# Kernel tuning notes

Hardware: AMD Instinct MI355X
Metric: run time of the kernel (lower is better)

The kernel has to match this reference:

```python
import jax, jax.numpy as jnp
import numpy as np

B, D, S, SE, H, DFF = 4, 1024, 1024, 1024, 16, 4096
DH = D // H
NUDGE = 1e-7


def norm(x):
    # x: [B, D, S]; custom layer norm: mean over (1,2), then divide by full L2 norm
    size = x.shape[1] * x.shape[2]
    mean = jnp.sum(x, axis=(1, 2)) / size
    x = x - mean[:, None, None]
    std = jnp.sqrt(jnp.sum(x * x, axis=(1, 2)))
    return x / (std[:, None, None] + NUDGE)


def mha(q_in, kv_in, Wq, Wk, Wv, Wo, causal):
    # q_in: [B, Sq, D], kv_in: [B, Sk, D]
    Bq, Sq, _ = q_in.shape
    Sk = kv_in.shape[1]
    q = (q_in @ Wq).reshape(Bq, Sq, H, DH)
    k = (kv_in @ Wk).reshape(Bq, Sk, H, DH)
    v = (kv_in @ Wv).reshape(Bq, Sk, H, DH)
    scores = jnp.einsum('bqhd,bkhd->bhqk', q, k) / jnp.sqrt(jnp.asarray(DH, q.dtype))
    if causal:
        mask = jnp.tril(jnp.ones((Sq, Sk), dtype=bool))
        scores = jnp.where(mask, scores, jnp.finfo(scores.dtype).min)
    attn = jax.nn.softmax(scores, axis=-1)
    out = jnp.einsum('bhqk,bkhd->bqhd', attn, v).reshape(Bq, Sq, D)
    return out @ Wo


def setup_inputs() -> dict:
    key = jax.random.key(0)
    ks = jax.random.split(key, 13)
    w = lambda k, sh: jax.random.normal(k, sh, dtype=jnp.float32) * 0.02
    return {
        'embedding': jax.random.normal(ks[0], (B, D, SE), dtype=jnp.float32),
        'other_inputs': jax.random.normal(ks[1], (B, D, S), dtype=jnp.float32),
        'Wq_s': w(ks[2], (D, D)), 'Wk_s': w(ks[3], (D, D)),
        'Wv_s': w(ks[4], (D, D)), 'Wo_s': w(ks[5], (D, D)),
        'Wq_c': w(ks[6], (D, D)), 'Wk_c': w(ks[7], (D, D)),
        'Wv_c': w(ks[8], (D, D)), 'Wo_c': w(ks[9], (D, D)),
        'W1': w(ks[10], (D, DFF)), 'b1': jnp.zeros((DFF,), jnp.float32),
        'W2': w(ks[11], (DFF, D)), 'b2': jnp.zeros((D,), jnp.float32),
    }


def reference(embedding, other_inputs, Wq_s, Wk_s, Wv_s, Wo_s,
              Wq_c, Wk_c, Wv_c, Wo_c, W1, b1, W2, b2):
    # tensors are [B, D, S]; attention operates on [B, S, D]
    x = other_inputs.transpose(0, 2, 1)
    sa = mha(x, x, Wq_s, Wk_s, Wv_s, Wo_s, causal=True)
    post_attention = norm(other_inputs + sa.transpose(0, 2, 1))

    pa = post_attention.transpose(0, 2, 1)
    emb = embedding.transpose(0, 2, 1)
    ca = mha(pa, emb, Wq_c, Wk_c, Wv_c, Wo_c, causal=False)
    post_embedding = norm(post_attention + ca.transpose(0, 2, 1))

    # per-token MLP (original loops over axis 2 and restacks; here fully batched)
    pe = post_embedding.transpose(0, 2, 1)  # [B, S, D]
    ff = jax.nn.relu(pe @ W1 + b1) @ W2 + b2
    return norm(post_embedding + ff.transpose(0, 2, 1))
```

## Files before the change

### kernel.cpp

```cpp
#include <hip/hip_runtime.h>
#include <cmath>

#define B_   4
#define D_   1024
#define S_   1024
#define H_   16
#define DH_  64
#define DFF_ 4096

typedef __attribute__((ext_vector_type(8))) short bf16x8;
typedef __attribute__((ext_vector_type(4))) float f32x4;

__device__ __forceinline__ unsigned short f2b(float f) {
    unsigned int u = __float_as_uint(f);
    u += 0x7fffu + ((u >> 16) & 1u);
    return (unsigned short)(u >> 16);
}

__device__ __forceinline__ void gload_lds16(const unsigned short* g, unsigned short* l) {
    __builtin_amdgcn_global_load_lds(
        (const __attribute__((address_space(1))) void*)g,
        (__attribute__((address_space(3))) void*)l, 16, 0, 0);
}

template <int BM, int BN, bool RES>
__global__ __launch_bounds__(256, 2)
void gemm_t(const unsigned short* __restrict__ A,
            const unsigned short* __restrict__ Wt,
            const float* __restrict__ bias,
            const float* __restrict__ residual,
            float* __restrict__ Cf, unsigned short* __restrict__ Cb,
            float* __restrict__ partial,
            int N, int K, int lda, int ldb, long csplit, int relu)
{
    constexpr int FM = BM / 32, FN = BN / 32;
    __shared__ unsigned short As[BM * 64];
    __shared__ unsigned short Bs[BN * 64];
    const int tid = threadIdx.x;
    const int w = tid >> 6, lane = tid & 63;
    const int quad = lane >> 4, l16 = lane & 15;
    const int m0 = blockIdx.x * BM, n0 = blockIdx.y * BN;
    const int wm = (w >> 1) * (BM / 2), wn = (w & 1) * (BN / 2);
    const int srow = lane >> 3;
    const int scol = ((lane & 7) ^ srow) * 8;

    A  += (size_t)blockIdx.z * K;
    Wt += (size_t)blockIdx.z * K;
    if (Cf) Cf += (size_t)blockIdx.z * csplit;

    f32x4 acc[FM][FN] = {};

    for (int k0 = 0; k0 < K; k0 += 64) {
#pragma unroll
        for (int i = 0; i < BM / 32; ++i) {
            const int inst = w + 4 * i;
            gload_lds16(A + (size_t)(m0 + inst * 8 + srow) * lda + k0 + scol,
                        As + inst * 512);
        }
#pragma unroll
        for (int i = 0; i < BN / 32; ++i) {
            const int inst = w + 4 * i;
            gload_lds16(Wt + (size_t)(n0 + inst * 8 + srow) * ldb + k0 + scol,
                        Bs + inst * 512);
        }
        __syncthreads();

#pragma unroll
        for (int kk = 0; kk < 2; ++kk) {
            bf16x8 af[FM], bfr[FN];
#pragma unroll
            for (int i = 0; i < FM; ++i) {
                const int r = wm + i * 16 + l16;
                af[i] = *(const bf16x8*)&As[r * 64 + (((kk * 4 + quad) ^ (r & 7)) * 8)];
            }
#pragma unroll
            for (int j = 0; j < FN; ++j) {
                const int r = wn + j * 16 + l16;
                bfr[j] = *(const bf16x8*)&Bs[r * 64 + (((kk * 4 + quad) ^ (r & 7)) * 8)];
            }
#pragma unroll
            for (int i = 0; i < FM; ++i)
#pragma unroll
                for (int j = 0; j < FN; ++j)
                    acc[i][j] = __builtin_amdgcn_mfma_f32_16x16x32_bf16(af[i], bfr[j], acc[i][j], 0, 0, 0);
        }
        __syncthreads();
    }

    float s = 0.f, ss = 0.f;
#pragma unroll
    for (int i = 0; i < FM; ++i) {
        const int grow = m0 + wm + i * 16 + quad * 4;
#pragma unroll
        for (int j = 0; j < FN; ++j) {
            const int gcol = n0 + wn + j * 16 + l16;
            const float bv = bias ? bias[gcol] : 0.f;
#pragma unroll
            for (int r = 0; r < 4; ++r) {
                float vv = acc[i][j][r] + bv;
                if (relu) vv = fmaxf(vv, 0.f);
                if constexpr (RES) {
                    vv += residual[(size_t)(grow + r) * N + gcol];
                    s += vv; ss += vv * vv;
                    Cf[(size_t)(grow + r) * N + gcol] = vv;
                } else {
                    if (Cf) Cf[(size_t)(grow + r) * N + gcol] = vv;
                    if (Cb) Cb[(size_t)(grow + r) * N + gcol] = f2b(vv);
                }
            }
        }
    }

    if constexpr (RES) {
        float* rs = (float*)As;
        float* rss = rs + 256;
        rs[tid] = s; rss[tid] = ss;
        __syncthreads();
        for (int off = 128; off > 0; off >>= 1) {
            if (tid < off) { rs[tid] += rs[tid + off]; rss[tid] += rss[tid + off]; }
            __syncthreads();
        }
        if (tid == 0) {
            constexpr int YPB = S_ / BM;
            const int b = blockIdx.x / YPB;
            const int chunk = (blockIdx.x % YPB) * gridDim.y + blockIdx.y;
            const int chunks = YPB * gridDim.y;
            partial[((size_t)b * chunks + chunk) * 2 + 0] = rs[0];
            partial[((size_t)b * chunks + chunk) * 2 + 1] = rss[0];
        }
    }
}

__global__ void reduce2_res(const float* __restrict__ pc, const float* __restrict__ res,
                            const float* __restrict__ bias, float* __restrict__ y,
                            float* __restrict__ partial)
{
    const size_t pcs = (size_t)4096 * 1024;
    const int b = blockIdx.y;
    const size_t base = (size_t)b * 1048576 + (size_t)blockIdx.x * 16384;
    float s = 0.f, ss = 0.f;
    for (int i = threadIdx.x; i < 4096; i += 256) {
        const size_t e = base + (size_t)i * 4;
        float4 v0 = *(const float4*)&pc[e];
        float4 v1 = *(const float4*)&pc[e + pcs];
        float4 rv = *(const float4*)&res[e];
        float4 bv = *(const float4*)&bias[e & 1023];
        float4 o;
        o.x = v0.x + v1.x + rv.x + bv.x;
        o.y = v0.y + v1.y + rv.y + bv.y;
        o.z = v0.z + v1.z + rv.z + bv.z;
        o.w = v0.w + v1.w + rv.w + bv.w;
        *(float4*)&y[e] = o;
        s += o.x + o.y + o.z + o.w;
        ss += o.x * o.x + o.y * o.y + o.z * o.z + o.w * o.w;
    }
    __shared__ float rs[256], rss[256];
    rs[threadIdx.x] = s; rss[threadIdx.x] = ss;
    __syncthreads();
    for (int off = 128; off > 0; off >>= 1) {
        if (threadIdx.x < off) {
            rs[threadIdx.x] += rs[threadIdx.x + off];
            rss[threadIdx.x] += rss[threadIdx.x + off];
        }
        __syncthreads();
    }
    if (threadIdx.x == 0) {
        partial[((size_t)b * 64 + blockIdx.x) * 2 + 0] = rs[0];
        partial[((size_t)b * 64 + blockIdx.x) * 2 + 1] = rss[0];
    }
}

__device__ __forceinline__ void stats_reduce(const float* __restrict__ partial,
                                             int b, int chunks, int tid,
                                             float* rs, float* rss,
                                             float& mean, float& inv)
{
    float s = 0.f, ss = 0.f;
    for (int i = tid; i < chunks; i += 256) {
        s  += partial[((size_t)b * chunks + i) * 2 + 0];
        ss += partial[((size_t)b * chunks + i) * 2 + 1];
    }
    rs[tid] = s; rss[tid] = ss;
    __syncthreads();
    for (int off = 128; off > 0; off >>= 1) {
        if (tid < off) { rs[tid] += rs[tid + off]; rss[tid] += rss[tid + off]; }
        __syncthreads();
    }
    const float size = (float)(D_ * S_);
    const float m = rs[0] / size;
    const float var = fmaxf(rss[0] - size * m * m, 0.f);
    mean = m;
    inv = 1.f / (sqrtf(var) + 1e-7f);
    __syncthreads();
}

__global__ void norm_apply_dual(float* __restrict__ y, unsigned short* __restrict__ yb,
                                const float* __restrict__ partial, int chunks)
{
    __shared__ float rs[256], rss[256];
    const int b = blockIdx.y;
    float mean, inv;
    stats_reduce(partial, b, chunks, threadIdx.x, rs, rss, mean, inv);

    const int perBatch = D_ * S_;
    float4* y4 = (float4*)(y + (size_t)b * perBatch);
    unsigned short* yb_ = yb + (size_t)b * perBatch;
    const int n4 = perBatch / 4;
    for (int i = blockIdx.x * blockDim.x + threadIdx.x; i < n4;
         i += gridDim.x * blockDim.x) {
        float4 v = y4[i];
        v.x = (v.x - mean) * inv; v.y = (v.y - mean) * inv;
        v.z = (v.z - mean) * inv; v.w = (v.w - mean) * inv;
        y4[i] = v;
        ushort4 hh; hh.x = f2b(v.x); hh.y = f2b(v.y); hh.z = f2b(v.z); hh.w = f2b(v.w);
        *(ushort4*)(yb_ + (size_t)i * 4) = hh;
    }
}

template <bool CAUSAL>
__global__ __launch_bounds__(256, 2)
void attn_mfma2(const unsigned short* __restrict__ q, const unsigned short* __restrict__ k,
                const unsigned short* __restrict__ vt, unsigned short* __restrict__ o,
                int qstride, int kstride)
{
    __shared__ unsigned short Ks[64][72];
    __shared__ unsigned short Vt[64][72];
    __shared__ unsigned short Ps[4][2][16][72];
    const int tid = threadIdx.x;
    const int w = tid >> 6, lane = tid & 63;
    const int quad = lane >> 4, l16 = lane & 15;
    const int h = blockIdx.y, b = blockIdx.z;
    const int qt = CAUSAL ? ((blockIdx.x + h) & 7) : blockIdx.x;
    const int q0 = qt * 128;

    const unsigned short* qA = q + (size_t)(b * S_ + q0 + w * 16 + l16) * qstride + h * DH_;
    const unsigned short* qB = qA + (size_t)64 * qstride;
    const bf16x8 qa0 = *(const bf16x8*)(qA + quad * 8);
    const bf16x8 qa1 = *(const bf16x8*)(qA + 32 + quad * 8);
    const bf16x8 qb0 = *(const bf16x8*)(qB + quad * 8);
    const bf16x8 qb1 = *(const bf16x8*)(qB + 32 + quad * 8);

    f32x4 OA[4] = {}, OB[4] = {};
    float lA[4] = {}, lB[4] = {};

    const int nblk = CAUSAL ? (2 * qt + 2) : (S_ / 64);
    for (int t = 0; t < nblk; ++t) {
        const int j0 = t * 64;
#pragma unroll
        for (int it = 0; it < 2; ++it) {
            const int id2 = tid + it * 256;
            const int row = id2 >> 3, c8 = (id2 & 7) * 8;
            *(bf16x8*)&Ks[row][c8] =
                *(const bf16x8*)(k + (size_t)(b * S_ + j0 + row) * kstride + h * DH_ + c8);
            *(bf16x8*)&Vt[row][c8] =
                *(const bf16x8*)(vt + (size_t)((b * H_ + h) * DH_ + row) * S_ + j0 + c8);
        }
        __syncthreads();

        const bool doA = !CAUSAL || (t <= 2 * qt);
        const bool diagA = CAUSAL && (t == 2 * qt);
        const bool diagB = CAUSAL && (t == 2 * qt + 1);

        f32x4 stA[4], stB[4];
#pragma unroll
        for (int n = 0; n < 4; ++n) {
            const bf16x8 kf0 = *(const bf16x8*)&Ks[n * 16 + l16][quad * 8];
            const bf16x8 kf1 = *(const bf16x8*)&Ks[n * 16 + l16][32 + quad * 8];
            if (doA) {
                f32x4 c = {};
                c = __builtin_amdgcn_mfma_f32_16x16x32_bf16(qa0, kf0, c, 0, 0, 0);
                c = __builtin_amdgcn_mfma_f32_16x16x32_bf16(qa1, kf1, c, 0, 0, 0);
                stA[n] = c;
            }
            f32x4 c = {};
            c = __builtin_amdgcn_mfma_f32_16x16x32_bf16(qb0, kf0, c, 0, 0, 0);
            c = __builtin_amdgcn_mfma_f32_16x16x32_bf16(qb1, kf1, c, 0, 0, 0);
            stB[n] = c;
        }

        if (doA) {
#pragma unroll
            for (int n = 0; n < 4; ++n)
#pragma unroll
                for (int r = 0; r < 4; ++r) {
                    float sv = stA[n][r] * 0.125f;
                    if (diagA) {
                        const int row = q0 + w * 16 + quad * 4 + r;
                        const int key = j0 + n * 16 + l16;
                        if (key > row) sv = -1e30f;
                    }
                    const float p = __expf(sv);
                    lA[r] += p;
                    Ps[w][0][quad * 4 + r][n * 16 + l16] = f2b(p);
                }
        }
#pragma unroll
        for (int n = 0; n < 4; ++n)
#pragma unroll
            for (int r = 0; r < 4; ++r) {
                float sv = stB[n][r] * 0.125f;
                if (diagB) {
                    const int row = q0 + 64 + w * 16 + quad * 4 + r;
                    const int key = j0 + n * 16 + l16;
                    if (key > row) sv = -1e30f;
                }
                const float p = __expf(sv);
                lB[r] += p;
                Ps[w][1][quad * 4 + r][n * 16 + l16] = f2b(p);
            }
        __threadfence_block();

        const bf16x8 pa0 = *(const bf16x8*)&Ps[w][0][l16][quad * 8];
        const bf16x8 pa1 = *(const bf16x8*)&Ps[w][0][l16][32 + quad * 8];
        const bf16x8 pb0 = *(const bf16x8*)&Ps[w][1][l16][quad * 8];
        const bf16x8 pb1 = *(const bf16x8*)&Ps[w][1][l16][32 + quad * 8];
#pragma unroll
        for (int n = 0; n < 4; ++n) {
            const bf16x8 vf0 = *(const bf16x8*)&Vt[n * 16 + l16][quad * 8];
            const bf16x8 vf1 = *(const bf16x8*)&Vt[n * 16 + l16][32 + quad * 8];
            if (doA) {
                OA[n] = __builtin_amdgcn_mfma_f32_16x16x32_bf16(pa0, vf0, OA[n], 0, 0, 0);
                OA[n] = __builtin_amdgcn_mfma_f32_16x16x32_bf16(pa1, vf1, OA[n], 0, 0, 0);
            }
            OB[n] = __builtin_amdgcn_mfma_f32_16x16x32_bf16(pb0, vf0, OB[n], 0, 0, 0);
            OB[n] = __builtin_amdgcn_mfma_f32_16x16x32_bf16(pb1, vf1, OB[n], 0, 0, 0);
        }
        __syncthreads();
    }

#pragma unroll
    for (int r = 0; r < 4; ++r) {
        float la = lA[r], lb = lB[r];
        la += __shfl_xor(la, 1); la += __shfl_xor(la, 2);
        la += __shfl_xor(la, 4); la += __shfl_xor(la, 8);
        lb += __shfl_xor(lb, 1); lb += __shfl_xor(lb, 2);
        lb += __shfl_xor(lb, 4); lb += __shfl_xor(lb, 8);
        const float ia = 1.f / la, ib = 1.f / lb;
        const size_t baseA = (size_t)(b * S_ + q0 + w * 16 + quad * 4 + r) * D_ + h * DH_;
        const size_t baseB = baseA + (size_t)64 * D_;
#pragma unroll
        for (int n = 0; n < 4; ++n) {
            o[baseA + n * 16 + l16] = f2b(OA[n][r] * ia);
            o[baseB + n * 16 + l16] = f2b(OB[n][r] * ib);
        }
    }
}

__global__ void transpose_v(const unsigned short* __restrict__ src,
                            unsigned short* __restrict__ dst, int istride)
{
    __shared__ unsigned short t[32][34];
    const int z = blockIdx.z, b = z >> 4, h = z & 15;
    const int s0 = blockIdx.x * 32, d0 = blockIdx.y * 32;
    const int tx = threadIdx.x, ty = threadIdx.y;
#pragma unroll
    for (int i = 0; i < 4; ++i)
        t[ty + i * 8][tx] =
            src[(size_t)(b * S_ + s0 + ty + i * 8) * istride + h * DH_ + d0 + tx];
    __syncthreads();
#pragma unroll
    for (int i = 0; i < 4; ++i)
        dst[(size_t)(z * DH_ + d0 + ty + i * 8) * S_ + s0 + tx] = t[tx][ty + i * 8];
}

struct WJob { const float* src; int sld; long doff; int dld; };
struct WJobs { WJob j[16]; };

__global__ void wtrans_all(WJobs js, unsigned short* __restrict__ dst)
{
    __shared__ float tile[32][33];
    const WJob J = js.j[blockIdx.z];
    const int c0 = blockIdx.x * 32, r0 = blockIdx.y * 32;
    const int tx = threadIdx.x, ty = threadIdx.y;
#pragma unroll
    for (int i = 0; i < 4; ++i)
        tile[ty + i * 8][tx] = J.src[(size_t)(r0 + ty + i * 8) * J.sld + c0 + tx];
    __syncthreads();
#pragma unroll
    for (int i = 0; i < 4; ++i)
        dst[J.doff + (size_t)(c0 + ty + i * 8) * J.dld + r0 + tx] =
            f2b(tile[tx][ty + i * 8]);
}

__global__ void transpose_in(const float* __restrict__ other, const float* __restrict__ emb,
                             float* __restrict__ f0, unsigned short* __restrict__ xb,
                             unsigned short* __restrict__ eb)
{
    __shared__ float tile[32][33];
    const int z = blockIdx.z;
    const int b = z & 3;
    const bool isEmb = z >= 4;
    const float* ip = (isEmb ? emb : other) + (size_t)b * 1048576;
    const int c0 = blockIdx.x * 32, r0 = blockIdx.y * 32;
    const int tx = threadIdx.x, ty = threadIdx.y;
#pragma unroll
    for (int i = 0; i < 4; ++i)
        tile[ty + i * 8][tx] = ip[(size_t)(r0 + ty + i * 8) * 1024 + c0 + tx];
    __syncthreads();
#pragma unroll
    for (int i = 0; i < 4; ++i) {
        const float v = tile[tx][ty + i * 8];
        const size_t oidx = (size_t)b * 1048576 + (size_t)(c0 + ty + i * 8) * 1024 + r0 + tx;
        if (isEmb) eb[oidx] = f2b(v);
        else { f0[oidx] = v; xb[oidx] = f2b(v); }
    }
}

__global__ void transpose_out(const float* __restrict__ in, float* __restrict__ outf,
                              const float* __restrict__ partial, int chunks)
{
    __shared__ float tile[32][33];
    __shared__ float rs[256], rss[256];
    const int z = blockIdx.z;
    const int tx = threadIdx.x, ty = threadIdx.y;
    const int tid = ty * 32 + tx;

    float mean, inv;
    stats_reduce(partial, z, chunks, tid, rs, rss, mean, inv);

    const float* ip = in + (size_t)z * 1048576;
    const int c0 = blockIdx.x * 32, r0 = blockIdx.y * 32;
#pragma unroll
    for (int i = 0; i < 4; ++i)
        tile[ty + i * 8][tx] = ip[(size_t)(r0 + ty + i * 8) * 1024 + c0 + tx];
    __syncthreads();
#pragma unroll
    for (int i = 0; i < 4; ++i) {
        const float v = (tile[tx][ty + i * 8] - mean) * inv;
        outf[(size_t)z * 1048576 + (size_t)(c0 + ty + i * 8) * 1024 + r0 + tx] = v;
    }
}

extern "C" void kernel_launch(void* const* d_in, const int* in_sizes, int n_in,
                              void* d_out, int out_size, void* d_ws, size_t ws_size,
                              hipStream_t stream)
{
    const float* embedding = (const float*)d_in[0];
    const float* other     = (const float*)d_in[1];
    const float* W1 = (const float*)d_in[10];
    const float* b1 = (const float*)d_in[11];
    const float* W2 = (const float*)d_in[12];
    const float* b2 = (const float*)d_in[13];
    float* out = (float*)d_out;

    char* wsb = (char*)d_ws;
    const size_t MB = 1u << 20;
    float* f0 = (float*)(wsb + 0 * MB);
    float* f2 = (float*)(wsb + 16 * MB);
    unsigned short* wts  = (unsigned short*)(wsb + 32 * MB);
    unsigned short* wqkv = wts;
    unsigned short* wo_s = wts + 3 * 1048576;
    unsigned short* wq_c = wts + 4 * 1048576;
    unsigned short* wkv_c= wts + 5 * 1048576;
    unsigned short* wo_c = wts + 7 * 1048576;
    unsigned short* w1t  = wts + 8 * 1048576;
    unsigned short* w2t  = wts + 12 * 1048576;
    unsigned short* actA = (unsigned short*)(wsb + 64 * MB);
    unsigned short* actB = (unsigned short*)(wsb + 72 * MB);
    unsigned short* actC = (unsigned short*)(wsb + 80 * MB);
    unsigned short* actC2 = actC + 4 * 1048576;
    unsigned short* aout  = actC + 12 * 1048576;
    float* pc      = (float*)(wsb + 112 * MB);
    float* partial = (float*)(wsb + 176 * MB);

    const dim3 blkT(32, 8), blk256(256);
    const dim3 gAttn(S_ / 128, H_, B_);
    const dim3 gVt(32, 2, B_ * H_);
    const dim3 gApply(64, B_);

    WJobs js;
    for (int z = 0; z < 8; ++z)
        js.j[z] = { (const float*)d_in[2 + z], 1024, (long)z * 1048576, 1024 };
    for (int q = 0; q < 4; ++q)
        js.j[8 + q] = { W1 + (size_t)q * 1024, 4096, (long)(8 + q) * 1048576, 1024 };
    for (int q = 0; q < 4; ++q)
        js.j[12 + q] = { W2 + (size_t)q * 1048576, 1024, 12L * 1048576 + q * 1024, 4096 };
    hipLaunchKernelGGL(wtrans_all, dim3(32, 32, 16), blkT, 0, stream, js, wts);

    hipLaunchKernelGGL(transpose_in, dim3(32, 32, 8), blkT, 0, stream,
                       other, embedding, f0, actA, actB);

    hipLaunchKernelGGL((gemm_t<128, 128, false>), dim3(32, 24), blk256, 0, stream,
                       actA, wqkv, nullptr, nullptr, nullptr, actC, nullptr,
                       3072, 1024, 1024, 1024, 0L, 0);
    hipLaunchKernelGGL(transpose_v, gVt, blkT, 0, stream, actC + 2048, actA, 3072);
    hipLaunchKernelGGL(attn_mfma2<true>, gAttn, blk256, 0, stream,
                       actC, actC + 1024, actA, aout, 3072, 3072);
    hipLaunchKernelGGL((gemm_t<64, 128, true>), dim3(64, 8), blk256, 0, stream,
                       aout, wo_s, nullptr, f0, f2, nullptr, partial,
                       1024, 1024, 1024, 1024, 0L, 0);
    hipLaunchKernelGGL(norm_apply_dual, gApply, blk256, 0, stream, f2, actA, partial, 128);

    hipLaunchKernelGGL((gemm_t<64, 128, false>), dim3(64, 8), blk256, 0, stream,
                       actA, wq_c, nullptr, nullptr, nullptr, actC, nullptr,
                       1024, 1024, 1024, 1024, 0L, 0);
    hipLaunchKernelGGL((gemm_t<128, 128, false>), dim3(32, 16), blk256, 0, stream,
                       actB, wkv_c, nullptr, nullptr, nullptr, actC2, nullptr,
                       2048, 1024, 1024, 1024, 0L, 0);
    hipLaunchKernelGGL(transpose_v, gVt, blkT, 0, stream, actC2 + 1024, actB, 2048);
    hipLaunchKernelGGL(attn_mfma2<false>, gAttn, blk256, 0, stream,
                       actC, actC2, actB, aout, 1024, 2048);
    hipLaunchKernelGGL((gemm_t<64, 128, true>), dim3(64, 8), blk256, 0, stream,
                       aout, wo_c, nullptr, f2, f0, nullptr, partial,
                       1024, 1024, 1024, 1024, 0L, 0);
    hipLaunchKernelGGL(norm_apply_dual, gApply, blk256, 0, stream, f0, actA, partial, 128);

    hipLaunchKernelGGL((gemm_t<128, 128, false>), dim3(32, 32), blk256, 0, stream,
                       actA, w1t, b1, nullptr, nullptr, actC, nullptr,
                       DFF_, 1024, 1024, 1024, 0L, 1);
    hipLaunchKernelGGL((gemm_t<128, 128, false>), dim3(32, 8, 2), blk256, 0, stream,
                       actC, w2t, nullptr, nullptr, pc, nullptr, nullptr,
                       1024, 2048, 4096, 4096, (long)4096 * 1024, 0);
    hipLaunchKernelGGL(reduce2_res, gApply, blk256, 0, stream, pc, f0, b2, f2, partial);
    hipLaunchKernelGGL(transpose_out, dim3(32, 32, B_), blkT, 0, stream, f2, out, partial, 64);

    (void)in_sizes; (void)n_in; (void)out_size; (void)ws_size;
}
```

Measured before the change: 514.2 us.

## Stage 128-key K/V tiles via direct global-to-LDS loads with XOR swizzle

The attention kernel now loads 128 keys per outer iteration instead of 64, using global_load_lds to write K and V^T straight into shared memory without going through registers. The LDS layouts drop row padding in favour of XOR swizzles to avoid bank conflicts. Each tile is processed as two 64-key sub-blocks, which halves the number of block-wide barriers per key range. In exchange, shared memory per block grows, and the causal path may do one extra half-tile of loads on the diagonal.

After: 500.9 us. 2.6% less time.

```diff
diff --git a/kernel.cpp b/kernel.cpp
--- a/kernel.cpp
+++ b/kernel.cpp
@@ -219,12 +219,12 @@
 
 template <bool CAUSAL>
 __global__ __launch_bounds__(256, 2)
-void attn_mfma2(const unsigned short* __restrict__ q, const unsigned short* __restrict__ k,
+void attn_mfma3(const unsigned short* __restrict__ q, const unsigned short* __restrict__ k,
                 const unsigned short* __restrict__ vt, unsigned short* __restrict__ o,
                 int qstride, int kstride)
 {
-    __shared__ unsigned short Ks[64][72];
-    __shared__ unsigned short Vt[64][72];
+    __shared__ unsigned short Ks[128 * 64];
+    __shared__ unsigned short Vt[64 * 128];
     __shared__ unsigned short Ps[4][2][16][72];
     const int tid = threadIdx.x;
     const int w = tid >> 6, lane = tid & 63;
@@ -233,6 +233,9 @@
     const int qt = CAUSAL ? ((blockIdx.x + h) & 7) : blockIdx.x;
     const int q0 = qt * 128;
 
+    const int ksr = lane >> 3, ksc = ((lane & 7) ^ (lane >> 3)) * 8;
+    const int vsr = lane >> 4, vsc = lane & 15;
+
     const unsigned short* qA = q + (size_t)(b * S_ + q0 + w * 16 + l16) * qstride + h * DH_;
     const unsigned short* qB = qA + (size_t)64 * qstride;
     const bf16x8 qa0 = *(const bf16x8*)(qA + quad * 8);
@@ -243,87 +246,95 @@
     f32x4 OA[4] = {}, OB[4] = {};
     float lA[4] = {}, lB[4] = {};
 
-    const int nblk = CAUSAL ? (2 * qt + 2) : (S_ / 64);
-    for (int t = 0; t < nblk; ++t) {
-        const int j0 = t * 64;
-#pragma unroll
-        for (int it = 0; it < 2; ++it) {
-            const int id2 = tid + it * 256;
-            const int row = id2 >> 3, c8 = (id2 & 7) * 8;
-            *(bf16x8*)&Ks[row][c8] =
-                *(const bf16x8*)(k + (size_t)(b * S_ + j0 + row) * kstride + h * DH_ + c8);
-            *(bf16x8*)&Vt[row][c8] =
-                *(const bf16x8*)(vt + (size_t)((b * H_ + h) * DH_ + row) * S_ + j0 + c8);
-        }
-        __syncthreads();
-
-        const bool doA = !CAUSAL || (t <= 2 * qt);
-        const bool diagA = CAUSAL && (t == 2 * qt);
-        const bool diagB = CAUSAL && (t == 2 * qt + 1);
-
-        f32x4 stA[4], stB[4];
-#pragma unroll
-        for (int n = 0; n < 4; ++n) {
-            const bf16x8 kf0 = *(const bf16x8*)&Ks[n * 16 + l16][quad * 8];
-            const bf16x8 kf1 = *(const bf16x8*)&Ks[n * 16 + l16][32 + quad * 8];
+    const int nit = CAUSAL ? (qt + 1) : (S_ / 128);
+    for (int t = 0; t < nit; ++t) {
+        const int j0 = t * 128;
+#pragma unroll
+        for (int i = 0; i < 4; ++i) {
+            const int ins = w + 4 * i;
+            gload_lds16(k + (size_t)(b * S_ + j0 + ins * 8 + ksr) * kstride + h * DH_ + ksc,
+                        Ks + ins * 512);
+            const int vrow = ins * 4 + vsr;
+            gload_lds16(vt + (size_t)((b * H_ + h) * DH_ + vrow) * S_ + j0
+                           + ((vsc ^ (vrow & 15)) * 8),
+                        Vt + ins * 512);
+        }
+        __syncthreads();
+
+#pragma unroll
+        for (int g = 0; g < 2; ++g) {
+            const int kb = 2 * t + g;
+            const int jg = j0 + g * 64;
+            const bool doA = !CAUSAL || (kb <= 2 * qt);
+            const bool diagA = CAUSAL && (kb == 2 * qt);
+            const bool diagB = CAUSAL && (kb == 2 * qt + 1);
+
+            f32x4 stA[4], stB[4];
+#pragma unroll
+            for (int n = 0; n < 4; ++n) {
+                const int kr = g * 64 + n * 16 + l16;
+                const bf16x8 kf0 = *(const bf16x8*)&Ks[kr * 64 + ((quad ^ (kr & 7)) * 8)];
+                const bf16x8 kf1 = *(const bf16x8*)&Ks[kr * 64 + (((quad + 4) ^ (kr & 7)) * 8)];
+                if (doA) {
+                    f32x4 c = {};
+                    c = __builtin_amdgcn_mfma_f32_16x16x32_bf16(qa0, kf0, c, 0, 0, 0);
+                    c = __builtin_amdgcn_mfma_f32_16x16x32_bf16(qa1, kf1, c, 0, 0, 0);
+                    stA[n] = c;
+                }
+                f32x4 c = {};
+                c = __builtin_amdgcn_mfma_f32_16x16x32_bf16(qb0, kf0, c, 0, 0, 0);
+                c = __builtin_amdgcn_mfma_f32_16x16x32_bf16(qb1, kf1, c, 0, 0, 0);
+                stB[n] = c;
+            }
+
             if (doA) {
-                f32x4 c = {};
-                c = __builtin_amdgcn_mfma_f32_16x16x32_bf16(qa0, kf0, c, 0, 0, 0);
-                c = __builtin_amdgcn_mfma_f32_16x16x32_bf16(qa1, kf1, c, 0, 0, 0);
-                stA[n] = c;
+#pragma unroll
+                for (int n = 0; n < 4; ++n)
+#pragma unroll
+                    for (int r = 0; r < 4; ++r) {
+                        float sv = stA[n][r] * 0.125f;
+                        if (diagA) {
+                            const int row = q0 + w * 16 + quad * 4 + r;
+                            const int key = jg + n * 16 + l16;
+                            if (key > row) sv = -1e30f;
+                        }
+                        const float p = __expf(sv);
+                        lA[r] += p;
+                        Ps[w][0][quad * 4 + r][n * 16 + l16] = f2b(p);
+                    }
             }
-            f32x4 c = {};
-            c = __builtin_amdgcn_mfma_f32_16x16x32_bf16(qb0, kf0, c, 0, 0, 0);
-            c = __builtin_amdgcn_mfma_f32_16x16x32_bf16(qb1, kf1, c, 0, 0, 0);
-            stB[n] = c;
-        }
-
-        if (doA) {
 #pragma unroll
             for (int n = 0; n < 4; ++n)
 #pragma unroll
                 for (int r = 0; r < 4; ++r) {
-                    float sv = stA[n][r] * 0.125f;
-                    if (diagA) {
-                        const int row = q0 + w * 16 + quad * 4 + r;
-                        const int key = j0 + n * 16 + l16;
+                    float sv = stB[n][r] * 0.125f;
+                    if (diagB) {
+                        const int row = q0 + 64 + w * 16 + quad * 4 + r;
+                        const int key = jg + n * 16 + l16;
                         if (key > row) sv = -1e30f;
                     }
                     const float p = __expf(sv);
-                    lA[r] += p;
-                    Ps[w][0][quad * 4 + r][n * 16 + l16] = f2b(p);
+                    lB[r] += p;
+                    Ps[w][1][quad * 4 + r][n * 16 + l16] = f2b(p);
                 }
-        }
-#pragma unroll
-        for (int n = 0; n < 4; ++n)
-#pragma unroll
-            for (int r = 0; r < 4; ++r) {
-                float sv = stB[n][r] * 0.125f;
-                if (diagB) {
-                    const int row = q0 + 64 + w * 16 + quad * 4 + r;
-                    const int key = j0 + n * 16 + l16;
-                    if (key > row) sv = -1e30f;
+            __threadfence_block();
+
+            const bf16x8 pa0 = *(const bf16x8*)&Ps[w][0][l16][quad * 8];
+            const bf16x8 pa1 = *(const bf16x8*)&Ps[w][0][l16][32 + quad * 8];
+            const bf16x8 pb0 = *(const bf16x8*)&Ps[w][1][l16][quad * 8];
+            const bf16x8 pb1 = *(const bf16x8*)&Ps[w][1][l16][32 + quad * 8];
+#pragma unroll
+            for (int n = 0; n < 4; ++n) {
+                const int vr = n * 16 + l16;
+                const bf16x8 vf0 = *(const bf16x8*)&Vt[vr * 128 + (((g * 8 + quad) ^ l16) * 8)];
+                const bf16x8 vf1 = *(const bf16x8*)&Vt[vr * 128 + (((g * 8 + quad + 4) ^ l16) * 8)];
+                if (doA) {
+                    OA[n] = __builtin_amdgcn_mfma_f32_16x16x32_bf16(pa0, vf0, OA[n], 0, 0, 0);
+                    OA[n] = __builtin_amdgcn_mfma_f32_16x16x32_bf16(pa1, vf1, OA[n], 0, 0, 0);
                 }
-                const float p = __expf(sv);
-                lB[r] += p;
-                Ps[w][1][quad * 4 + r][n * 16 + l16] = f2b(p);
+                OB[n] = __builtin_amdgcn_mfma_f32_16x16x32_bf16(pb0, vf0, OB[n], 0, 0, 0);
+                OB[n] = __builtin_amdgcn_mfma_f32_16x16x32_bf16(pb1, vf1, OB[n], 0, 0, 0);
             }
-        __threadfence_block();
-
-        const bf16x8 pa0 = *(const bf16x8*)&Ps[w][0][l16][quad * 8];
-        const bf16x8 pa1 = *(const bf16x8*)&Ps[w][0][l16][32 + quad * 8];
-        const bf16x8 pb0 = *(const bf16x8*)&Ps[w][1][l16][quad * 8];
-        const bf16x8 pb1 = *(const bf16x8*)&Ps[w][1][l16][32 + quad * 8];
-#pragma unroll
-        for (int n = 0; n < 4; ++n) {
-            const bf16x8 vf0 = *(const bf16x8*)&Vt[n * 16 + l16][quad * 8];
-            const bf16x8 vf1 = *(const bf16x8*)&Vt[n * 16 + l16][32 + quad * 8];
-            if (doA) {
-                OA[n] = __builtin_amdgcn_mfma_f32_16x16x32_bf16(pa0, vf0, OA[n], 0, 0, 0);
-                OA[n] = __builtin_amdgcn_mfma_f32_16x16x32_bf16(pa1, vf1, OA[n], 0, 0, 0);
-            }
-            OB[n] = __builtin_amdgcn_mfma_f32_16x16x32_bf16(pb0, vf0, OB[n], 0, 0, 0);
-            OB[n] = __builtin_amdgcn_mfma_f32_16x16x32_bf16(pb1, vf1, OB[n], 0, 0, 0);
         }
         __syncthreads();
     }
@@ -484,7 +495,7 @@
                        actA, wqkv, nullptr, nullptr, nullptr, actC, nullptr,
                        3072, 1024, 1024, 1024, 0L, 0);
     hipLaunchKernelGGL(transpose_v, gVt, blkT, 0, stream, actC + 2048, actA, 3072);
-    hipLaunchKernelGGL(attn_mfma2<true>, gAttn, blk256, 0, stream,
+    hipLaunchKernelGGL(attn_mfma3<true>, gAttn, blk256, 0, stream,
                        actC, actC + 1024, actA, aout, 3072, 3072);
     hipLaunchKernelGGL((gemm_t<64, 128, true>), dim3(64, 8), blk256, 0, stream,
                        aout, wo_s, nullptr, f0, f2, nullptr, partial,
@@ -498,7 +509,7 @@
                        actB, wkv_c, nullptr, nullptr, nullptr, actC2, nullptr,
                        2048, 1024, 1024, 1024, 0L, 0);
     hipLaunchKernelGGL(transpose_v, gVt, blkT, 0, stream, actC2 + 1024, actB, 2048);
-    hipLaunchKernelGGL(attn_mfma2<false>, gAttn, blk256, 0, stream,
+    hipLaunchKernelGGL(attn_mfma3<false>, gAttn, blk256, 0, stream,
                        actC, actC2, actB, aout, 1024, 2048);
     hipLaunchKernelGGL((gemm_t<64, 128, true>), dim3(64, 8), blk256, 0, stream,
                        aout, wo_c, nullptr, f2, f0, nullptr, partial,
```
